# Kernel optimization log

Measured on AMD Instinct MI355X. Metric: run time of the kernel, lower is better.

The kernel has to match this reference:

```python
import jax, jax.numpy as jnp
import numpy as np

B, T, D, H, CL = 2, 4096, 2048, 16, 512
DK = D // H          # key_dim == head_dim (value_factor=1) == 128
SCALING = DK ** -0.5


def _rel_pos():
    # RetNet relative position: per-head decay gamma, rotary sin/cos, chunk decay masks
    h = np.arange(H, dtype=np.float64)
    gamma = 1.0 - 2.0 ** (-5.0 - h)                           # (H,)
    angle = 1.0 / (10000.0 ** (np.arange(0, DK, 2) / DK))
    angle = np.repeat(angle, 2)                               # (DK,) each freq duplicated
    pos = np.arange(T)[:, None] * angle[None, :]              # (T, DK)
    sin, cos = np.sin(pos), np.cos(pos)
    idx = np.arange(CL)
    expn = idx[:, None] - idx[None, :]                        # (CL, CL)
    m = np.where(expn >= 0, gamma[:, None, None] ** np.maximum(expn, 0), 0.0)  # (H,CL,CL)
    scale = np.sqrt(m.sum(-1, keepdims=True))                 # (H,CL,1)
    mask = m / scale
    cross_decay = (gamma ** CL)[:, None, None]                # (H,1,1)
    inner = gamma[:, None] ** (idx + 1)                       # (H,CL)
    inner_decay = inner[:, :, None] / (scale / mask[:, -1].sum(-1)[:, None, None])  # (H,CL,1)
    f32 = lambda a: jnp.asarray(a, jnp.float32)
    return f32(sin), f32(cos), f32(mask), f32(cross_decay), f32(inner_decay)


def setup_inputs() -> dict:
    key = jax.random.key(0)
    kx, kq, kk, kv, kg, ko = jax.random.split(key, 6)
    sin, cos, mask, cross_decay, inner_decay = _rel_pos()
    mk = lambda k: jax.random.normal(k, (D, D), jnp.float32) * 0.02  # ~xavier w/ small gain
    z = jnp.zeros((D,), jnp.float32)
    return dict(
        x=jax.random.normal(kx, (B, T, D), jnp.float32),
        sin=sin, cos=cos, mask=mask, cross_decay=cross_decay, inner_decay=inner_decay,
        wq=mk(kq), bq=z, wk=mk(kk), bk=z, wv=mk(kv), bv=z, wg=mk(kg), bg=z,
        wo=jax.random.normal(ko, (D, D), jnp.float32) * (1.0 / np.sqrt(D)), bo=z,
    )


def _rotate_every_two(x):
    x1, x2 = x[..., ::2], x[..., 1::2]
    return jnp.stack((-x2, x1), axis=-1).reshape(x.shape)


def _theta_shift(x, sin, cos):
    return x * cos + _rotate_every_two(x) * sin


def reference(x, sin, cos, mask, cross_decay, inner_decay,
              wq, bq, wk, bk, wv, bv, wg, bg, wo, bo):
    NC = T // CL
    q = (x @ wq.T + bq).reshape(B, T, H, DK).transpose(0, 2, 1, 3)           # (B,H,T,DK)
    k = ((x @ wk.T + bk) * SCALING).reshape(B, T, H, DK).transpose(0, 2, 1, 3)
    v = x @ wv.T + bv                                                        # (B,T,D)
    g = x @ wg.T + bg
    qr = _theta_shift(q, sin, cos)
    kr = _theta_shift(k, sin, cos)
    # chunk views -> (B, NC, H, CL, DK)
    qr = qr.reshape(B, H, NC, CL, DK).transpose(0, 2, 1, 3, 4)
    kr = kr.reshape(B, H, NC, CL, DK).transpose(0, 2, 1, 3, 4)
    vc = v.reshape(B, NC, CL, H, DK).transpose(0, 1, 3, 2, 4)                # (B,NC,H,CL,HD)
    # intra-chunk decay-masked attention
    qk = jnp.einsum('bnhld,bnhmd->bnhlm', qr, kr) * mask                      # (B,NC,H,CL,CL)
    inner_scale = jnp.clip(jnp.abs(jax.lax.stop_gradient(qk)).sum(-1, keepdims=True), 1.0)
    inner_out = jnp.einsum('bnhlm,bnhmd->bnhld', qk / inner_scale, vc)
    # per-chunk KV contribution (keys weighted by remaining decay = last mask row)
    kv = jnp.einsum('bnhlk,bnhld->bnhkd', kr, vc * mask[:, -1, :, None])      # (B,NC,H,DK,HD)

    def step(carry, kv_i):
        kv_state, kv_scale = carry
        out = (kv_state / kv_scale, kv_scale)
        new_state = kv_state * cross_decay + kv_i
        s = jnp.abs(jax.lax.stop_gradient(new_state)).sum(-2, keepdims=True)
        new_scale = jnp.clip(s.max(-1, keepdims=True), 1.0)
        return (new_state, new_scale), out

    init = (jnp.zeros((B, H, DK, DK), x.dtype), jnp.ones((B, H, 1, 1), x.dtype))
    _, (kv_rec, cross_scale) = jax.lax.scan(step, init, jnp.moveaxis(kv, 1, 0))
    kv_rec = jnp.moveaxis(kv_rec, 0, 1)            # (B,NC,H,DK,HD)
    cross_scale = jnp.moveaxis(cross_scale, 0, 1)  # (B,NC,H,1,1)
    all_scale = jnp.maximum(inner_scale, cross_scale)
    cross_out = jnp.einsum('bnhlk,bnhkd->bnhld', qr * inner_decay, kv_rec)
    out = inner_out / (all_scale / inner_scale) + cross_out / (all_scale / cross_scale)
    out = out.transpose(0, 1, 3, 2, 4)             # (B,NC,CL,H,HD)
    # group_norm: LayerNorm over head_dim, no affine, eps=1e-6
    mu = out.mean(-1, keepdims=True)
    var = ((out - mu) ** 2).mean(-1, keepdims=True)
    out = (out - mu) / jnp.sqrt(var + 1e-6)
    out = out.reshape(B, T, D)
    out = jax.nn.silu(g) * out                     # swish gate
    return out @ wo.T + bo
```

## Files before the change

### kernel.cpp

```cpp
#include <hip/hip_runtime.h>
#include <hip/hip_bf16.h>
#include <math.h>

#define NB   2
#define NT   4096
#define ND   2048
#define NH   16
#define NDK  128
#define NCL  512
#define NNC  8
#define NTOK 8192
#define SCALING 0.08838834764831845f

typedef unsigned short u16;
typedef short short8 __attribute__((ext_vector_type(8)));
typedef unsigned short ushort8 __attribute__((ext_vector_type(8)));
typedef float f32x4 __attribute__((ext_vector_type(4)));
typedef float float4v __attribute__((ext_vector_type(4)));
typedef short short4v __attribute__((ext_vector_type(4)));

__device__ __forceinline__ float bf2f(u16 u) {
    union { unsigned int i; float f; } v; v.i = ((unsigned int)u) << 16; return v.f;
}
__device__ __forceinline__ u16 f2bf(float f) {
    union { float f; unsigned int i; } v; v.f = f;
    unsigned int r = v.i + 0x7FFFu + ((v.i >> 16) & 1u);
    return (u16)(r >> 16);
}

__device__ __forceinline__ void gload16(const void* g, void* l) {
    __builtin_amdgcn_global_load_lds(
        (const __attribute__((address_space(1))) unsigned int*)g,
        (__attribute__((address_space(3))) unsigned int*)l, 16, 0, 0);
}

#define MFMA16(acc_, a_, b_) acc_ = __builtin_amdgcn_mfma_f32_16x16x32_bf16(a_, b_, acc_, 0, 0, 0)
#define SBAR  asm volatile("s_barrier" ::: "memory")


__device__ __forceinline__ void stage_half(const u16* __restrict__ g, int ld,
                                           u16* lds, int tid)
{
#pragma unroll
    for (int j = 0; j < 2; ++j) {
        int c = tid + j * 512;
        int row = c >> 3, u = c & 7;
        gload16(g + (size_t)row * ld + ((u ^ (row & 7)) * 8), lds + (size_t)c * 8);
    }
}

__device__ __forceinline__ void tile_nb(
    int G, int nkt,
    const u16* Aop, const u16* Bop, int ld,
    int tid, int arow, int brow, int uc0, int uc1,
    u16* ARd, u16* BRd, u16* AWr, u16* BWr,
    f32x4 acc[8][4])
{
    if (G + 1 < nkt) {
        const u16* Ag = Aop + (size_t)(G + 1) * 64;
        const u16* Bg = Bop + (size_t)(G + 1) * 64;
        stage_half(Ag,                    ld, AWr,        tid);
        stage_half(Ag + (size_t)128 * ld, ld, AWr + 8192, tid);
        stage_half(Bg,                    ld, BWr,        tid);
        stage_half(Bg + (size_t)128 * ld, ld, BWr + 8192, tid);
    }

    short8 a[4][2], bA[2][2], bB[2][2];

#pragma unroll
    for (int mf = 0; mf < 4; ++mf) {
        a[mf][0] = *(const short8*)(ARd + (size_t)(arow + mf * 16) * 64 + uc0);
        a[mf][1] = *(const short8*)(ARd + (size_t)(arow + mf * 16) * 64 + uc1);
    }
#pragma unroll
    for (int nf = 0; nf < 2; ++nf) {
        bA[nf][0] = *(const short8*)(BRd + (size_t)(brow + nf * 16) * 64 + uc0);
        bA[nf][1] = *(const short8*)(BRd + (size_t)(brow + nf * 16) * 64 + uc1);
    }
    __builtin_amdgcn_s_setprio(1);
#pragma unroll
    for (int mf = 0; mf < 4; ++mf)
#pragma unroll
        for (int nf = 0; nf < 2; ++nf) {
            MFMA16(acc[mf][nf], a[mf][0], bA[nf][0]);
            MFMA16(acc[mf][nf], a[mf][1], bA[nf][1]);
        }
    __builtin_amdgcn_s_setprio(0);

#pragma unroll
    for (int nf = 0; nf < 2; ++nf) {
        bB[nf][0] = *(const short8*)(BRd + (size_t)(brow + 32 + nf * 16) * 64 + uc0);
        bB[nf][1] = *(const short8*)(BRd + (size_t)(brow + 32 + nf * 16) * 64 + uc1);
    }
    __builtin_amdgcn_s_setprio(1);
#pragma unroll
    for (int mf = 0; mf < 4; ++mf)
#pragma unroll
        for (int nf = 0; nf < 2; ++nf) {
            MFMA16(acc[mf][2 + nf], a[mf][0], bB[nf][0]);
            MFMA16(acc[mf][2 + nf], a[mf][1], bB[nf][1]);
        }
    __builtin_amdgcn_s_setprio(0);

#pragma unroll
    for (int mf = 0; mf < 4; ++mf) {
        a[mf][0] = *(const short8*)(ARd + (size_t)(arow + 64 + mf * 16) * 64 + uc0);
        a[mf][1] = *(const short8*)(ARd + (size_t)(arow + 64 + mf * 16) * 64 + uc1);
    }
    __builtin_amdgcn_s_setprio(1);
#pragma unroll
    for (int mf = 0; mf < 4; ++mf)
#pragma unroll
        for (int nf = 0; nf < 2; ++nf) {
            MFMA16(acc[4 + mf][2 + nf], a[mf][0], bB[nf][0]);
            MFMA16(acc[4 + mf][2 + nf], a[mf][1], bB[nf][1]);
        }
    __builtin_amdgcn_s_setprio(0);

    __builtin_amdgcn_s_setprio(1);
#pragma unroll
    for (int mf = 0; mf < 4; ++mf)
#pragma unroll
        for (int nf = 0; nf < 2; ++nf) {
            MFMA16(acc[4 + mf][nf], a[mf][0], bA[nf][0]);
            MFMA16(acc[4 + mf][nf], a[mf][1], bA[nf][1]);
        }
    __builtin_amdgcn_s_setprio(0);

    asm volatile("s_waitcnt vmcnt(0) lgkmcnt(0)" ::: "memory");
    SBAR;
}

__device__ __forceinline__ void gemm256_core(
    const u16* Aop, const u16* Bop,
    int ld, int nkt,
    u16* A0, u16* A1, u16* B0, u16* B1, f32x4 acc[8][4])
{
    const int tid  = threadIdx.x;
    const int lane = tid & 63;
    const int lr   = lane & 15;
    const int lg   = lane >> 4;
    const int wid  = tid >> 6;
    const int wm   = wid >> 2;
    const int wn   = wid & 3;

    const int swz  = lr & 7;
    const int uc0  = ((0 * 4 + lg) ^ swz) * 8;
    const int uc1  = ((1 * 4 + lg) ^ swz) * 8;
    const int arow = wm * 128 + lr;
    const int brow = wn * 64 + lr;

    stage_half(Aop,                    ld, A0,        tid);
    stage_half(Aop + (size_t)128 * ld, ld, A0 + 8192, tid);
    stage_half(Bop,                    ld, B0,        tid);
    stage_half(Bop + (size_t)128 * ld, ld, B0 + 8192, tid);
    asm volatile("s_waitcnt vmcnt(0)" ::: "memory");
    SBAR;

    for (int G = 0; G < nkt; G += 2) {
        tile_nb(G,     nkt, Aop, Bop, ld, tid, arow, brow, uc0, uc1,
                A0, B0, A1, B1, acc);
        tile_nb(G + 1, nkt, Aop, Bop, ld, tid, arow, brow, uc0, uc1,
                A1, B1, A0, B0, acc);
    }
}

__device__ __forceinline__ void gemm_bt_core(
    const u16* __restrict__ A, const u16* __restrict__ Bm,
    int lda, int ldb, int K, u16* As, u16* Bs, f32x4 acc[4][4])
{
    const int tid  = threadIdx.x;
    const int lane = tid & 63;
    const int lr   = lane & 15;
    const int lg   = lane >> 4;
    const int wid  = tid >> 6;
    const int wr   = (wid >> 1) * 64;
    const int wc   = (wid & 1) * 64;
    for (int kt = 0; kt < K; kt += 64) {
#pragma unroll
        for (int i = 0; i < 4; ++i) {
            int c = tid + i * 256;
            int row = c >> 3, col = (c & 7) * 8;
            gload16(A  + (size_t)row * lda + kt + col, (char*)As + (size_t)c * 16);
            gload16(Bm + (size_t)row * ldb + kt + col, (char*)Bs + (size_t)c * 16);
        }
        __syncthreads();
#pragma unroll
        for (int kk = 0; kk < 2; ++kk) {
            short8 a[4], b[4];
#pragma unroll
            for (int m = 0; m < 4; ++m)
                a[m] = *(const short8*)(As + (wr + m * 16 + lr) * 64 + kk * 32 + lg * 8);
#pragma unroll
            for (int n = 0; n < 4; ++n)
                b[n] = *(const short8*)(Bs + (wc + n * 16 + lr) * 64 + kk * 32 + lg * 8);
#pragma unroll
            for (int m = 0; m < 4; ++m)
#pragma unroll
                for (int n = 0; n < 4; ++n)
                    acc[m][n] = __builtin_amdgcn_mfma_f32_16x16x32_bf16(a[m], b[n], acc[m][n], 0, 0, 0);
        }
        __syncthreads();
    }
}

__global__ __launch_bounds__(256) void k_f2bf(const float* __restrict__ src,
                                              u16* __restrict__ dst, int n4)
{
    int i = blockIdx.x * blockDim.x + threadIdx.x;
    int stride = gridDim.x * blockDim.x;
    for (int j = i; j < n4; j += stride) {
        float4v f = *(const float4v*)(src + (size_t)j * 4);
        short4v o;
        o.x = (short)f2bf(f.x); o.y = (short)f2bf(f.y);
        o.z = (short)f2bf(f.z); o.w = (short)f2bf(f.w);
        *(short4v*)(dst + (size_t)j * 4) = o;
    }
}

__global__ __launch_bounds__(512, 2) void k_gemm1(
    const u16* __restrict__ xb, const u16* __restrict__ wb,
    const float* __restrict__ bq, const float* __restrict__ bk,
    const float* __restrict__ bv, const float* __restrict__ bg,
    const float* __restrict__ sinp, const float* __restrict__ cosp,
    const float* __restrict__ maskp,
    u16* __restrict__ qro, u16* __restrict__ kro, u16* __restrict__ krwT,
    u16* __restrict__ vT, u16* __restrict__ glin)
{
    __shared__ __align__(16) u16 A0[256 * 64];
    __shared__ __align__(16) u16 A1[256 * 64];
    __shared__ __align__(16) u16 B0[256 * 64];
    __shared__ __align__(16) u16 B1[256 * 64];
    f32x4 acc[8][4];
#pragma unroll
    for (int m = 0; m < 8; ++m)
#pragma unroll
        for (int n = 0; n < 4; ++n) acc[m][n] = (f32x4){0.f, 0.f, 0.f, 0.f};

    int bid = blockIdx.x;
    int swzb = (bid & 7) * 128 + (bid >> 3);
    int mt = swzb >> 5, nt = swzb & 31;

    gemm256_core(xb + (size_t)mt * 256 * ND, wb + (size_t)nt * 256 * ND,
                 ND, ND / 64, A0, A1, B0, B1, acc);

    int tid = threadIdx.x, lane = tid & 63, lr = lane & 15, lg = lane >> 4, wid = tid >> 6;
    int wm = wid >> 2, wn = wid & 3;
    int which = nt >> 3;

    if (which <= 1) {
        const float* bias = (which == 0) ? bq : bk;
#pragma unroll
        for (int mf = 0; mf < 8; ++mf) {
#pragma unroll
            for (int nf = 0; nf < 4; ++nf) {
#pragma unroll
                for (int r = 0; r < 4; ++r) {
                    int row = mt * 256 + wm * 128 + mf * 16 + lg * 4 + r;
                    int col = nt * 256 + wn * 64 + nf * 16 + lr;
                    int f = col & 2047, h = f >> 7, d = f & 127;
                    int b = row >> 12, t = row & 4095, cn = t >> 9, cl = t & 511;
                    float v = acc[mf][nf][r] + bias[f];
                    if (which == 1) v *= SCALING;
                    float sv = sinp[(size_t)t * NDK + d];
                    float cv = cosp[(size_t)t * NDK + d];
                    float vp = __shfl_xor(v, 1);
                    float rot = (lr & 1) ? vp : -vp;
                    float o = v * cv + rot * sv;
                    size_t chbase = (size_t)(b * NNC + cn) * NH + h;
                    if (which == 0) {
                        qro[(chbase * NCL + cl) * NDK + d] = f2bf(o);
                    } else {
                        kro[(chbase * NCL + cl) * NDK + d] = f2bf(o);
                        float w = maskp[((size_t)h * NCL + (NCL - 1)) * NCL + cl];
                        krwT[(chbase * NDK + d) * NCL + cl] = f2bf(o * w);
                    }
                }
            }
        }
    } else {
#pragma unroll
        for (int mf = 0; mf < 8; ++mf) {
#pragma unroll
            for (int nf = 0; nf < 4; ++nf) {
#pragma unroll
                for (int r = 0; r < 4; ++r) {
                    int row = mt * 256 + wm * 128 + mf * 16 + lg * 4 + r;
                    int col = nt * 256 + wn * 64 + nf * 16 + lr;
                    int f = col & 2047;
                    float v = acc[mf][nf][r];
                    if (which == 2) {
                        int h = f >> 7, d = f & 127;
                        int b = row >> 12, t = row & 4095, cn = t >> 9, cl = t & 511;
                        vT[(((size_t)(b * NNC + cn) * NH + h) * NDK + d) * NCL + cl] = f2bf(v + bv[f]);
                    } else {
                        glin[(size_t)row * ND + f] = f2bf(v + bg[f]);
                    }
                }
            }
        }
    }
}

__global__ __launch_bounds__(512, 2) void k_gemm2(
    const u16* __restrict__ y, const u16* __restrict__ wob,
    const float* __restrict__ bo, float* __restrict__ out)
{
    __shared__ __align__(16) u16 A0[256 * 64];
    __shared__ __align__(16) u16 A1[256 * 64];
    __shared__ __align__(16) u16 B0[256 * 64];
    __shared__ __align__(16) u16 B1[256 * 64];
    f32x4 acc[8][4];
#pragma unroll
    for (int m = 0; m < 8; ++m)
#pragma unroll
        for (int n = 0; n < 4; ++n) acc[m][n] = (f32x4){0.f, 0.f, 0.f, 0.f};

    int bid = blockIdx.x;
    int swzb = (bid & 7) * 32 + (bid >> 3);
    int mt = swzb >> 3, nt = swzb & 7;

    gemm256_core(y + (size_t)mt * 256 * ND, wob + (size_t)nt * 256 * ND,
                 ND, ND / 64, A0, A1, B0, B1, acc);

    int tid = threadIdx.x, lane = tid & 63, lr = lane & 15, lg = lane >> 4, wid = tid >> 6;
    int wm = wid >> 2, wn = wid & 3;
#pragma unroll
    for (int mf = 0; mf < 8; ++mf)
#pragma unroll
        for (int nf = 0; nf < 4; ++nf)
#pragma unroll
            for (int r = 0; r < 4; ++r) {
                int row = mt * 256 + wm * 128 + mf * 16 + lg * 4 + r;
                int col = nt * 256 + wn * 64 + nf * 16 + lr;
                out[(size_t)row * ND + col] = acc[mf][nf][r] + bo[col];
            }
}

__global__ __launch_bounds__(256) void k_inner(
    const u16* __restrict__ qr, const u16* __restrict__ kr,
    const u16* __restrict__ vT, const float* __restrict__ mask,
    float* __restrict__ iraw, float* __restrict__ iscale)
{
    __shared__ __align__(16) u16 Qs[128 * 128];
    __shared__ __align__(16) u16 Ks[32 * 128];
    __shared__ __align__(16) u16 Vs[128 * 32];
    __shared__ __align__(16) u16 Ps[4][32 * 32];
    __shared__ float sl[128];

    int qt = blockIdx.x, bnh = blockIdx.y;
    int h = bnh & 15;
    const u16* Q = qr + (size_t)bnh * NCL * NDK + (size_t)qt * 128 * NDK;
    const u16* K = kr + (size_t)bnh * NCL * NDK;
    const u16* V = vT + (size_t)bnh * NDK * NCL;
    const float* M = mask + (size_t)h * NCL * NCL + (size_t)qt * 128 * NCL;

    int tid = threadIdx.x, lane = tid & 63, lr = lane & 15, lg = lane >> 4, wid = tid >> 6;
    if (tid < 128) sl[tid] = 0.f;
#pragma unroll
    for (int i = 0; i < 8; ++i) {
        int c = tid + i * 256;
        gload16(Q + (size_t)c * 8, (char*)Qs + (size_t)c * 16);
    }
    __syncthreads();

    short8 aq[2][4];
#pragma unroll
    for (int i = 0; i < 2; ++i)
#pragma unroll
        for (int kk = 0; kk < 4; ++kk)
            aq[i][kk] = *(const short8*)(Qs + (wid * 32 + i * 16 + lr) * 128 + kk * 32 + lg * 8);

    f32x4 acc[2][8];
#pragma unroll
    for (int i = 0; i < 2; ++i)
#pragma unroll
        for (int n = 0; n < 8; ++n) acc[i][n] = (f32x4){0.f, 0.f, 0.f, 0.f};

    int msteps = qt * 4 + 4;
    for (int ms = 0; ms < msteps; ++ms) {
        int mb = ms * 32;
#pragma unroll
        for (int i = 0; i < 2; ++i) {
            int c = tid + i * 256;
            int row = c >> 4, cc = (c & 15) * 8;
            gload16(K + (size_t)(mb + row) * NDK + cc, (char*)Ks + (size_t)c * 16);
        }
#pragma unroll
        for (int i = 0; i < 2; ++i) {
            int c = tid + i * 256;
            int row = c >> 2, cc = (c & 3) * 8;
            gload16(V + (size_t)row * NCL + mb + cc, (char*)Vs + (size_t)c * 16);
        }
        __syncthreads();

        f32x4 pa[2][2];
#pragma unroll
        for (int i = 0; i < 2; ++i) { pa[i][0] = (f32x4){0.f,0.f,0.f,0.f}; pa[i][1] = (f32x4){0.f,0.f,0.f,0.f}; }
#pragma unroll
        for (int kk = 0; kk < 4; ++kk) {
            short8 bk0 = *(const short8*)(Ks + (lr) * 128 + kk * 32 + lg * 8);
            short8 bk1 = *(const short8*)(Ks + (16 + lr) * 128 + kk * 32 + lg * 8);
#pragma unroll
            for (int i = 0; i < 2; ++i) {
                pa[i][0] = __builtin_amdgcn_mfma_f32_16x16x32_bf16(aq[i][kk], bk0, pa[i][0], 0, 0, 0);
                pa[i][1] = __builtin_amdgcn_mfma_f32_16x16x32_bf16(aq[i][kk], bk1, pa[i][1], 0, 0, 0);
            }
        }
#pragma unroll
        for (int i = 0; i < 2; ++i) {
#pragma unroll
            for (int r = 0; r < 4; ++r) {
                int rloc = i * 16 + lg * 4 + r;
                int row128 = wid * 32 + rloc;
                float m0 = M[(size_t)row128 * NCL + mb + lr];
                float m1 = M[(size_t)row128 * NCL + mb + 16 + lr];
                float p0 = pa[i][0][r] * m0;
                float p1 = pa[i][1][r] * m1;
                float ss = fabsf(p0) + fabsf(p1);
                ss += __shfl_xor(ss, 1); ss += __shfl_xor(ss, 2);
                ss += __shfl_xor(ss, 4); ss += __shfl_xor(ss, 8);
                if (lr == 0) sl[row128] += ss;
                Ps[wid][rloc * 32 + lr]      = f2bf(p0);
                Ps[wid][rloc * 32 + 16 + lr] = f2bf(p1);
            }
        }
        __syncthreads();

        short8 ap[2];
#pragma unroll
        for (int i = 0; i < 2; ++i)
            ap[i] = *(const short8*)(Ps[wid] + (i * 16 + lr) * 32 + lg * 8);
#pragma unroll
        for (int n = 0; n < 8; ++n) {
            short8 bv8 = *(const short8*)(Vs + (n * 16 + lr) * 32 + lg * 8);
#pragma unroll
            for (int i = 0; i < 2; ++i)
                acc[i][n] = __builtin_amdgcn_mfma_f32_16x16x32_bf16(ap[i], bv8, acc[i][n], 0, 0, 0);
        }
        __syncthreads();
    }

    float* OR = iraw + ((size_t)bnh * NCL + (size_t)qt * 128) * NDK;
#pragma unroll
    for (int i = 0; i < 2; ++i)
#pragma unroll
        for (int n = 0; n < 8; ++n)
#pragma unroll
            for (int r = 0; r < 4; ++r) {
                int row = wid * 32 + i * 16 + lg * 4 + r;
                int col = n * 16 + lr;
                OR[(size_t)row * NDK + col] = acc[i][n][r];
            }
    __syncthreads();
    if (tid < 128) iscale[(size_t)bnh * NCL + qt * 128 + tid] = fmaxf(1.f, sl[tid]);
}

__global__ __launch_bounds__(256) void k_kv(
    const u16* __restrict__ krwT, const u16* __restrict__ vT, float* __restrict__ kvi)
{
    __shared__ __align__(16) u16 As[128 * 64];
    __shared__ __align__(16) u16 Bs[128 * 64];
    f32x4 acc[4][4];
#pragma unroll
    for (int m = 0; m < 4; ++m)
#pragma unroll
        for (int n = 0; n < 4; ++n) acc[m][n] = (f32x4){0.f, 0.f, 0.f, 0.f};

    int bnh = blockIdx.x;
    gemm_bt_core(krwT + (size_t)bnh * NDK * NCL, vT + (size_t)bnh * NDK * NCL,
                 NCL, NCL, NCL, As, Bs, acc);

    int tid = threadIdx.x, lane = tid & 63, lr = lane & 15, lg = lane >> 4, wid = tid >> 6;
    int wr = (wid >> 1) * 64, wc = (wid & 1) * 64;
    float* O = kvi + (size_t)bnh * NDK * NDK;
#pragma unroll
    for (int m = 0; m < 4; ++m)
#pragma unroll
        for (int n = 0; n < 4; ++n)
#pragma unroll
            for (int r = 0; r < 4; ++r) {
                int row = wr + m * 16 + lg * 4 + r;
                int col = wc + n * 16 + lr;
                O[(size_t)row * NDK + col] = acc[m][n][r];
            }
}

__global__ __launch_bounds__(256) void k_scan(
    const float* __restrict__ kvi, const float* __restrict__ cdec,
    u16* __restrict__ kvrT, float* __restrict__ csc)
{
    int bh = blockIdx.x;
    int b = bh >> 4, h = bh & 15;
    float cd = cdec[h];
    int tid = threadIdx.x;
    int col = tid & 127;
    int r0 = (tid >> 7) * 64;
    float st[64];
#pragma unroll
    for (int i = 0; i < 64; ++i) st[i] = 0.f;
    float scale = 1.f;
    __shared__ float cs[128];
    __shared__ float scsh;

    for (int n = 0; n < NNC; ++n) {
        size_t idx = (size_t)((b * NNC + n) * NH + h);
        size_t kb = idx * (NDK * NDK);
        float inv = 1.f / scale;
#pragma unroll
        for (int i = 0; i < 64; ++i)
            kvrT[kb + (size_t)col * NDK + r0 + i] = f2bf(st[i] * inv);
        if (tid == 0) csc[idx] = scale;

        const float* KV = kvi + kb;
        float colsum = 0.f;
#pragma unroll
        for (int i = 0; i < 64; ++i) {
            float xv = st[i] * cd + KV[(size_t)(r0 + i) * NDK + col];
            st[i] = xv;
            colsum += fabsf(xv);
        }
        __syncthreads();
        if (tid < 128) cs[tid] = 0.f;
        __syncthreads();
        atomicAdd(&cs[col], colsum);
        __syncthreads();
        if (tid == 0) {
            float mx = cs[0];
            for (int i = 1; i < 128; ++i) mx = fmaxf(mx, cs[i]);
            scsh = fmaxf(1.f, mx);
        }
        __syncthreads();
        scale = scsh;
    }
}

__global__ __launch_bounds__(256) void k_combine(
    const u16* __restrict__ qr, const u16* __restrict__ kvrT,
    const float* __restrict__ iraw, const float* __restrict__ iscale,
    const float* __restrict__ cscale, const float* __restrict__ idecay,
    const u16* __restrict__ glin, u16* __restrict__ y)
{
    __shared__ __align__(16) u16 As[128 * 64];
    __shared__ __align__(16) u16 Bs[128 * 64];
    __shared__ float ssum[128];
    __shared__ float ssq[128];
    f32x4 acc[4][4];
#pragma unroll
    for (int m = 0; m < 4; ++m)
#pragma unroll
        for (int n = 0; n < 4; ++n) acc[m][n] = (f32x4){0.f, 0.f, 0.f, 0.f};

    int qt = blockIdx.x, bnh = blockIdx.y;
    int b = bnh >> 7, cn = (bnh >> 4) & 7, h = bnh & 15;
    gemm_bt_core(qr + (size_t)bnh * NCL * NDK + (size_t)qt * 128 * NDK,
                 kvrT + (size_t)bnh * NDK * NDK, NDK, NDK, NDK, As, Bs, acc);

    int tid = threadIdx.x, lane = tid & 63, lr = lane & 15, lg = lane >> 4, wid = tid >> 6;
    int wr = (wid >> 1) * 64, wc = (wid & 1) * 64;
    if (tid < 128) { ssum[tid] = 0.f; ssq[tid] = 0.f; }
    __syncthreads();
    float csv = cscale[bnh];

#pragma unroll
    for (int m = 0; m < 4; ++m) {
#pragma unroll
        for (int r = 0; r < 4; ++r) {
            int rloc = wr + m * 16 + lg * 4 + r;
            int l = qt * 128 + rloc;
            float isc = iscale[(size_t)bnh * NCL + l];
            float all = fmaxf(isc, csv);
            float c1 = 1.f / all;
            float c2 = (csv / all) * idecay[h * NCL + l];
            const float* ir = iraw + ((size_t)bnh * NCL + l) * NDK;
            float lsum = 0.f, lsq = 0.f;
#pragma unroll
            for (int n = 0; n < 4; ++n) {
                int col = wc + n * 16 + lr;
                float v = ir[col] * c1 + acc[m][n][r] * c2;
                acc[m][n][r] = v;
                lsum += v; lsq += v * v;
            }
            lsum += __shfl_xor(lsum, 1); lsum += __shfl_xor(lsum, 2);
            lsum += __shfl_xor(lsum, 4); lsum += __shfl_xor(lsum, 8);
            lsq  += __shfl_xor(lsq, 1);  lsq  += __shfl_xor(lsq, 2);
            lsq  += __shfl_xor(lsq, 4);  lsq  += __shfl_xor(lsq, 8);
            if (lr == 0) { atomicAdd(&ssum[rloc], lsum); atomicAdd(&ssq[rloc], lsq); }
        }
    }
    __syncthreads();
#pragma unroll
    for (int m = 0; m < 4; ++m) {
#pragma unroll
        for (int r = 0; r < 4; ++r) {
            int rloc = wr + m * 16 + lg * 4 + r;
            int l = qt * 128 + rloc;
            float mu = ssum[rloc] * (1.f / 128.f);
            float var = ssq[rloc] * (1.f / 128.f) - mu * mu;
            float rstd = rsqrtf(fmaxf(var, 0.f) + 1e-6f);
            int t = cn * NCL + l;
            size_t obase = ((size_t)(b * NT + t)) * ND + (size_t)h * NDK;
#pragma unroll
            for (int n = 0; n < 4; ++n) {
                int col = wc + n * 16 + lr;
                float gv = bf2f(glin[obase + col]);
                float sg = gv / (1.f + expf(-gv));
                float ov = (acc[m][n][r] - mu) * rstd * sg;
                y[obase + col] = f2bf(ov);
            }
        }
    }
}

extern "C" void kernel_launch(void* const* d_in, const int* in_sizes, int n_in,
                              void* d_out, int out_size, void* d_ws, size_t ws_size,
                              hipStream_t stream)
{
    const float* x    = (const float*)d_in[0];
    const float* sinp = (const float*)d_in[1];
    const float* cosp = (const float*)d_in[2];
    const float* mask = (const float*)d_in[3];
    const float* cdec = (const float*)d_in[4];
    const float* idec = (const float*)d_in[5];
    const float* wq   = (const float*)d_in[6];
    const float* bq   = (const float*)d_in[7];
    const float* wk   = (const float*)d_in[8];
    const float* bk   = (const float*)d_in[9];
    const float* wv   = (const float*)d_in[10];
    const float* bv   = (const float*)d_in[11];
    const float* wg   = (const float*)d_in[12];
    const float* bg   = (const float*)d_in[13];
    const float* wo   = (const float*)d_in[14];
    const float* bo   = (const float*)d_in[15];
    float* out = (float*)d_out;

    char* ws = (char*)d_ws;
    u16*   XB   = (u16*)(ws + 0);
    u16*   WB   = (u16*)(ws + 33554432);
    u16*   WOB  = (u16*)(ws + 67108864);
    u16*   QR   = (u16*)(ws + 75497472);
    u16*   KR   = (u16*)(ws + 109051904);
    u16*   KRWT = (u16*)(ws + 142606336);
    u16*   VT   = (u16*)(ws + 176160768);
    u16*   GLIN = (u16*)(ws + 209715200);
    float* KVI  = (float*)(ws + 243269632);
    float* CSC  = (float*)(ws + 260046848);
    float* IRAW = (float*)(ws + 0);
    u16*   Y    = KR;
    u16*   KVRT = KRWT;
    float* ISC  = (float*)(ws + 243269632);

    k_f2bf<<<2048, 256, 0, stream>>>(x, XB, 4194304);
    k_f2bf<<<1024, 256, 0, stream>>>(wq, WB,            1048576);
    k_f2bf<<<1024, 256, 0, stream>>>(wk, WB + 4194304,  1048576);
    k_f2bf<<<1024, 256, 0, stream>>>(wv, WB + 8388608,  1048576);
    k_f2bf<<<1024, 256, 0, stream>>>(wg, WB + 12582912, 1048576);
    k_f2bf<<<1024, 256, 0, stream>>>(wo, WOB,           1048576);

    k_gemm1<<<1024, 512, 0, stream>>>(XB, WB, bq, bk, bv, bg, sinp, cosp, mask,
                                      QR, KR, KRWT, VT, GLIN);
    k_kv<<<256, 256, 0, stream>>>(KRWT, VT, KVI);
    k_scan<<<32, 256, 0, stream>>>(KVI, cdec, KVRT, CSC);
    k_inner<<<dim3(4, 256), 256, 0, stream>>>(QR, KR, VT, mask, IRAW, ISC);
    k_combine<<<dim3(4, 256), 256, 0, stream>>>(QR, KVRT, IRAW, ISC, CSC, idec, GLIN, Y);
    k_gemm2<<<256, 512, 0, stream>>>(Y, WOB, bo, out);
}
```

Measured before the change: 878.0 us.

## Fuse cross-chunk attention, scale combine and group-norm gating into inner kernel

The separate combine kernel is removed. The inner-chunk attention kernel now also computes the cross-chunk product Q·KV directly from registers (reusing the Q fragments already loaded), combines it with the inner result using the scales, applies group norm and the swish gate, and writes the gated output in place into the gate buffer. This avoids writing and re-reading the fp32 inner-output buffer, the separate iscale buffer, and a kernel launch. The cost is higher register pressure in k_inner and uncached global reads of KV fragments. Reading sl at that point may also lack a barrier after the final loop.

```diff
diff --git a/kernel.cpp b/kernel.cpp
--- a/kernel.cpp
+++ b/kernel.cpp
@@ -340,7 +340,8 @@
 __global__ __launch_bounds__(256) void k_inner(
     const u16* __restrict__ qr, const u16* __restrict__ kr,
     const u16* __restrict__ vT, const float* __restrict__ mask,
-    float* __restrict__ iraw, float* __restrict__ iscale)
+    const u16* __restrict__ kvrT, const float* __restrict__ cscale,
+    const float* __restrict__ idecay, u16* __restrict__ glin)
 {
     __shared__ __align__(16) u16 Qs[128 * 128];
     __shared__ __align__(16) u16 Ks[32 * 128];
@@ -349,7 +350,7 @@
     __shared__ float sl[128];
 
     int qt = blockIdx.x, bnh = blockIdx.y;
-    int h = bnh & 15;
+    int b = bnh >> 7, cn = (bnh >> 4) & 7, h = bnh & 15;
     const u16* Q = qr + (size_t)bnh * NCL * NDK + (size_t)qt * 128 * NDK;
     const u16* K = kr + (size_t)bnh * NCL * NDK;
     const u16* V = vT + (size_t)bnh * NDK * NCL;
@@ -441,19 +442,63 @@
         __syncthreads();
     }
 
-    float* OR = iraw + ((size_t)bnh * NCL + (size_t)qt * 128) * NDK;
+    float csv = cscale[bnh];
+    const u16* KVR = kvrT + (size_t)bnh * NDK * NDK;
+
+    f32x4 acc2[2][8];
 #pragma unroll
     for (int i = 0; i < 2; ++i)
 #pragma unroll
-        for (int n = 0; n < 8; ++n)
-#pragma unroll
-            for (int r = 0; r < 4; ++r) {
-                int row = wid * 32 + i * 16 + lg * 4 + r;
+        for (int n = 0; n < 8; ++n) acc2[i][n] = (f32x4){0.f, 0.f, 0.f, 0.f};
+#pragma unroll
+    for (int n = 0; n < 8; ++n) {
+        short8 bk4[4];
+#pragma unroll
+        for (int kk = 0; kk < 4; ++kk)
+            bk4[kk] = *(const short8*)(KVR + (size_t)(n * 16 + lr) * NDK + kk * 32 + lg * 8);
+#pragma unroll
+        for (int kk = 0; kk < 4; ++kk)
+#pragma unroll
+            for (int i = 0; i < 2; ++i)
+                acc2[i][n] = __builtin_amdgcn_mfma_f32_16x16x32_bf16(aq[i][kk], bk4[kk], acc2[i][n], 0, 0, 0);
+    }
+
+#pragma unroll
+    for (int i = 0; i < 2; ++i) {
+#pragma unroll
+        for (int r = 0; r < 4; ++r) {
+            int row128 = wid * 32 + i * 16 + lg * 4 + r;
+            int l = qt * 128 + row128;
+            float isc = fmaxf(1.f, sl[row128]);
+            float all = fmaxf(isc, csv);
+            float c1 = 1.f / all;
+            float c2 = (csv / all) * idecay[h * NCL + l];
+            float v[8];
+            float lsum = 0.f, lsq = 0.f;
+#pragma unroll
+            for (int n = 0; n < 8; ++n) {
+                v[n] = acc[i][n][r] * c1 + acc2[i][n][r] * c2;
+                lsum += v[n]; lsq += v[n] * v[n];
+            }
+            lsum += __shfl_xor(lsum, 1); lsum += __shfl_xor(lsum, 2);
+            lsum += __shfl_xor(lsum, 4); lsum += __shfl_xor(lsum, 8);
+            lsq  += __shfl_xor(lsq, 1);  lsq  += __shfl_xor(lsq, 2);
+            lsq  += __shfl_xor(lsq, 4);  lsq  += __shfl_xor(lsq, 8);
+            float mu = lsum * (1.f / 128.f);
+            float var = lsq * (1.f / 128.f) - mu * mu;
+            float rstd = rsqrtf(fmaxf(var, 0.f) + 1e-6f);
+            int t = cn * NCL + l;
+            size_t obase = ((size_t)(b * NT + t)) * ND + (size_t)h * NDK;
+#pragma unroll
+            for (int n = 0; n < 8; ++n) {
                 int col = n * 16 + lr;
-                OR[(size_t)row * NDK + col] = acc[i][n][r];
-            }
-    __syncthreads();
-    if (tid < 128) iscale[(size_t)bnh * NCL + qt * 128 + tid] = fmaxf(1.f, sl[tid]);
+                float gv = bf2f(glin[obase + col]);
+                float sg = gv / (1.f + expf(-gv));
+                float ov = (v[n] - mu) * rstd * sg;
+                glin[obase + col] = f2bf(ov);
+            }
+        }
+    }
 }
 
 __global__ __launch_bounds__(256) void k_kv(
@@ -532,83 +577,6 @@
         }
         __syncthreads();
         scale = scsh;
-    }
-}
-
-__global__ __launch_bounds__(256) void k_combine(
-    const u16* __restrict__ qr, const u16* __restrict__ kvrT,
-    const float* __restrict__ iraw, const float* __restrict__ iscale,
-    const float* __restrict__ cscale, const float* __restrict__ idecay,
-    const u16* __restrict__ glin, u16* __restrict__ y)
-{
-    __shared__ __align__(16) u16 As[128 * 64];
-    __shared__ __align__(16) u16 Bs[128 * 64];
-    __shared__ float ssum[128];
-    __shared__ float ssq[128];
-    f32x4 acc[4][4];
-#pragma unroll
-    for (int m = 0; m < 4; ++m)
-#pragma unroll
-        for (int n = 0; n < 4; ++n) acc[m][n] = (f32x4){0.f, 0.f, 0.f, 0.f};
-
-    int qt = blockIdx.x, bnh = blockIdx.y;
-    int b = bnh >> 7, cn = (bnh >> 4) & 7, h = bnh & 15;
-    gemm_bt_core(qr + (size_t)bnh * NCL * NDK + (size_t)qt * 128 * NDK,
-                 kvrT + (size_t)bnh * NDK * NDK, NDK, NDK, NDK, As, Bs, acc);
-
-    int tid = threadIdx.x, lane = tid & 63, lr = lane & 15, lg = lane >> 4, wid = tid >> 6;
-    int wr = (wid >> 1) * 64, wc = (wid & 1) * 64;
-    if (tid < 128) { ssum[tid] = 0.f; ssq[tid] = 0.f; }
-    __syncthreads();
-    float csv = cscale[bnh];
-
-#pragma unroll
-    for (int m = 0; m < 4; ++m) {
-#pragma unroll
-        for (int r = 0; r < 4; ++r) {
-            int rloc = wr + m * 16 + lg * 4 + r;
-            int l = qt * 128 + rloc;
-            float isc = iscale[(size_t)bnh * NCL + l];
-            float all = fmaxf(isc, csv);
-            float c1 = 1.f / all;
-            float c2 = (csv / all) * idecay[h * NCL + l];
-            const float* ir = iraw + ((size_t)bnh * NCL + l) * NDK;
-            float lsum = 0.f, lsq = 0.f;
-#pragma unroll
-            for (int n = 0; n < 4; ++n) {
-                int col = wc + n * 16 + lr;
-                float v = ir[col] * c1 + acc[m][n][r] * c2;
-                acc[m][n][r] = v;
-                lsum += v; lsq += v * v;
-            }
-            lsum += __shfl_xor(lsum, 1); lsum += __shfl_xor(lsum, 2);
-            lsum += __shfl_xor(lsum, 4); lsum += __shfl_xor(lsum, 8);
-            lsq  += __shfl_xor(lsq, 1);  lsq  += __shfl_xor(lsq, 2);
-            lsq  += __shfl_xor(lsq, 4);  lsq  += __shfl_xor(lsq, 8);
-            if (lr == 0) { atomicAdd(&ssum[rloc], lsum); atomicAdd(&ssq[rloc], lsq); }
-        }
-    }
-    __syncthreads();
-#pragma unroll
-    for (int m = 0; m < 4; ++m) {
-#pragma unroll
-        for (int r = 0; r < 4; ++r) {
-            int rloc = wr + m * 16 + lg * 4 + r;
-            int l = qt * 128 + rloc;
-            float mu = ssum[rloc] * (1.f / 128.f);
-            float var = ssq[rloc] * (1.f / 128.f) - mu * mu;
-            float rstd = rsqrtf(fmaxf(var, 0.f) + 1e-6f);
-            int t = cn * NCL + l;
-            size_t obase = ((size_t)(b * NT + t)) * ND + (size_t)h * NDK;
-#pragma unroll
-            for (int n = 0; n < 4; ++n) {
-                int col = wc + n * 16 + lr;
-                float gv = bf2f(glin[obase + col]);
-                float sg = gv / (1.f + expf(-gv));
-                float ov = (acc[m][n][r] - mu) * rstd * sg;
-                y[obase + col] = f2bf(ov);
-            }
-        }
     }
 }
 
@@ -645,10 +613,7 @@
     u16*   GLIN = (u16*)(ws + 209715200);
     float* KVI  = (float*)(ws + 243269632);
     float* CSC  = (float*)(ws + 260046848);
-    float* IRAW = (float*)(ws + 0);
-    u16*   Y    = KR;
     u16*   KVRT = KRWT;
-    float* ISC  = (float*)(ws + 243269632);
 
     k_f2bf<<<2048, 256, 0, stream>>>(x, XB, 4194304);
     k_f2bf<<<1024, 256, 0, stream>>>(wq, WB,            1048576);
@@ -661,7 +626,6 @@
                                       QR, KR, KRWT, VT, GLIN);
     k_kv<<<256, 256, 0, stream>>>(KRWT, VT, KVI);
     k_scan<<<32, 256, 0, stream>>>(KVI, cdec, KVRT, CSC);
-    k_inner<<<dim3(4, 256), 256, 0, stream>>>(QR, KR, VT, mask, IRAW, ISC);
-    k_combine<<<dim3(4, 256), 256, 0, stream>>>(QR, KVRT, IRAW, ISC, CSC, idec, GLIN, Y);
-    k_gemm2<<<256, 512, 0, stream>>>(Y, WOB, bo, out);
-}
+    k_inner<<<dim3(4, 256), 256, 0, stream>>>(QR, KR, VT, mask, KVRT, CSC, idec, GLIN);
+    k_gemm2<<<256, 512, 0, stream>>>(GLIN, WOB, bo, out);
+}
```

Result: slower. 987.4 us (+12.5%).
